# Performance work log

Measured on AMD Instinct MI355X. Metric: run time of the kernel, lower is better.

The kernel has to match this reference:

```python
import jax, jax.numpy as jnp
import numpy as np

NEG = -1e30  # log-space 'zero' (stand-in for log(0))


def setup_inputs() -> dict:
    key = jax.random.key(0)
    k1, k2 = jax.random.split(key)
    K, Tp1, Y = 4, 513, 256  # K feature fns, T+1 transition steps, Y labels
    f = jax.random.normal(k1, (K, Tp1, Y, Y), dtype=jnp.float32)
    w = jax.random.uniform(k2, (K,), dtype=jnp.float32)
    return {"f": f, "w": w}


def _crf_core(f, w):
    # logM[t] = sum_k w_k * f[k, t]  (log of the original M before exp)
    K, Tp1, Y, _ = f.shape
    T = Tp1 - 1
    logM = jnp.einsum('k,ktij->tij', w, f)  # [T+1, Y, Y]
    # Boundary masking (original zeros M[0,1:,:] and M[T,:,1:]):
    is0 = (jnp.arange(Y) == 0)
    logM = logM.at[0].set(jnp.where(is0[:, None], logM[0], NEG))
    logM = logM.at[T].set(jnp.where(is0[None, :], logM[T], NEG))

    # log-alpha forward scan (stable log-space form of alpha[i+1] = alpha[i] @ M[i])
    la0 = jnp.where(is0, 0.0, NEG)  # alpha[0] one-hot at label 0
    def fwd_step(la, lm):
        la_new = jax.nn.logsumexp(la[:, None] + lm, axis=0)
        return la_new, la_new
    _, las = jax.lax.scan(fwd_step, la0, logM)
    log_alpha = jnp.concatenate([la0[None], las], axis=0)  # [T+2, Y]

    # log-beta backward scan (beta[i] = M[i] @ beta[i+1])
    lbT = jnp.where(is0, 0.0, NEG)  # beta[T+1] one-hot at label 0
    def bwd_step(lb, lm):
        lb_new = jax.nn.logsumexp(lm + lb[None, :], axis=1)
        return lb_new, lb_new
    _, lbs = jax.lax.scan(bwd_step, lbT, logM, reverse=True)
    log_beta = jnp.concatenate([lbs, lbT[None]], axis=0)  # [T+2, Y]

    logZ = jax.nn.logsumexp(log_alpha[T + 1])
    # pairwise posterior p(y_{i}=y', y_{i+1}=y | x) = alpha_i * M_i * beta_{i+1} / Z
    p12 = jnp.exp(log_alpha[:-1][:, :, None] + logM + log_beta[1:][:, None, :] - logZ)
    return p12, logM


def _viterbi(logM):
    # delta[0] = logM[0, 0]; delta[i] = max_{y'} delta[i-1][y'] + logM[i][y', y]
    T = logM.shape[0] - 1
    def vit_step(d, lm):
        scores = d[:, None] + lm  # [Y, Y]
        return jnp.max(scores, axis=0), jnp.argmax(scores, axis=0)
    dT, idxs = jax.lax.scan(vit_step, logM[0, 0], logM[1:T])
    last = jnp.argmax(dT)
    def back_step(y, idx):
        yp = idx[y]
        return yp, yp
    _, prevs = jax.lax.scan(back_step, last, idxs, reverse=True)
    return jnp.concatenate([prevs, last[None]])  # [T]


def reference(f, w):
    p12, logM = _crf_core(f, w)
    path = _viterbi(logM)
    return p12, path
```

## Files before the change

kernel.cpp:

```cpp
#include <hip/hip_runtime.h>

#define NEGV (-1e30f)
#define NM   ((size_t)513*65536)
#define NF4  (NM/4)

typedef _Float16 h2 __attribute__((ext_vector_type(2)));

#if defined(__has_builtin)
#if __has_builtin(__builtin_amdgcn_fdot2)
#define HAS_FDOT2 1
#endif
#endif

__device__ __forceinline__ float dot2f(h2 a, h2 b, float c){
#ifdef HAS_FDOT2
  return __builtin_amdgcn_fdot2(a, b, c, false);
#else
  return c + (float)a.x*(float)b.x + (float)a.y*(float)b.y;
#endif
}

__device__ __forceinline__ h2 u2h2(unsigned u){ return __builtin_bit_cast(h2, u); }

struct WS {
  float *fA, *fB, *fD, *fLZ;
  _Float16 *hA, *hB;
  unsigned char* idx8;
  unsigned long long *flagF8, *flagB8;
  int *flagV, *ctr;
};
__device__ __forceinline__ WS get_ws(void* w){
  WS s;
  float* f = (float*)w;
  s.fA  = f;
  s.fB  = f + 131584;
  s.fD  = s.fB + 131584;
  s.fLZ = s.fD + 131072;
  s.hA  = (_Float16*)(s.fLZ + 64);
  s.hB  = s.hA + 131584;
  s.idx8 = (unsigned char*)(s.hB + 131584);
  s.flagF8 = (unsigned long long*)(s.idx8 + 131072);
  s.flagB8 = s.flagF8 + 576;
  s.flagV  = (int*)(s.flagB8 + 576);
  s.ctr    = s.flagV + 576;
  return s;
}

__device__ __forceinline__ float block_max256(float v, float* sred){
  #pragma unroll
  for (int m2=32;m2>0;m2>>=1) v = fmaxf(v, __shfl_xor(v, m2, 64));
  if ((threadIdx.x & 63)==0) sred[threadIdx.x>>6] = v;
  __syncthreads();
  return fmaxf(fmaxf(sred[0],sred[1]), fmaxf(sred[2],sred[3]));
}
__device__ __forceinline__ float block_sum256(float v, float* sred){
  #pragma unroll
  for (int m2=32;m2>0;m2>>=1) v += __shfl_xor(v, m2, 64);
  if ((threadIdx.x & 63)==0) sred[4+(threadIdx.x>>6)] = v;
  __syncthreads();
  return sred[4]+sred[5]+sred[6]+sred[7];
}

__global__ __launch_bounds__(1024) void k0_init(void* wsv){
  WS s = get_ws(wsv);
  const int tid = threadIdx.x;
  for (int i=tid;i<576;i+=1024){ s.flagF8[i]=0ull; s.flagB8[i]=0ull; s.flagV[i]=0; }
  if (tid < 64) s.ctr[tid] = 0;
  __syncthreads();
  if (tid < 256){
    s.fA[tid] = (tid==0)?0.0f:NEGV;
    s.hA[tid] = (tid==0)?(_Float16)1.0f:(_Float16)0.0f;
    s.fB[(size_t)513*256+tid] = (tid==0)?0.0f:NEGV;
    s.hB[(size_t)513*256+tid] = (tid==0)?(_Float16)1.0f:(_Float16)0.0f;
  }
  if (tid==0){ s.flagF8[0] = (1ull<<32); s.flagB8[513] = (1ull<<32); }
}

__global__ __launch_bounds__(1024) void k1_logM(const float* __restrict__ f,
                                                const float* __restrict__ w,
                                                float* __restrict__ lm, void* wsv){
  WS s = get_ws(wsv);
  const float w0=w[0], w1=w[1], w2=w[2], w3=w[3];
  const float4* f0=(const float4*)f;
  const float4* f1=f0+NF4; const float4* f2=f1+NF4; const float4* f3=f2+NF4;
  float4* o=(float4*)lm;
  for (size_t i=(size_t)blockIdx.x*1024+threadIdx.x; i<NF4; i+=(size_t)gridDim.x*1024){
    float4 a=f0[i], b=f1[i], c=f2[i], d=f3[i];
    float4 v;
    v.x = w0*a.x+w1*b.x+w2*c.x+w3*d.x;
    v.y = w0*a.y+w1*b.y+w2*c.y+w3*d.y;
    v.z = w0*a.z+w1*b.z+w2*c.z+w3*d.z;
    v.w = w0*a.w+w1*b.w+w2*c.w+w3*d.w;
    size_t e=i*4;
    int t=(int)(e>>16), r=(int)((e>>8)&255), cc=(int)(e&255);
    if (t==0 && r!=0){ v.x=NEGV; v.y=NEGV; v.z=NEGV; v.w=NEGV; }
    if (t==512){ if (cc!=0) v.x=NEGV; v.y=NEGV; v.z=NEGV; v.w=NEGV; }
    o[i]=v;
  }
  if (blockIdx.x==0 && threadIdx.x<256){
    int j=threadIdx.x;
    float sv = w0*f[j] + w1*f[NM+j] + w2*f[2*NM+j] + w3*f[3*NM+j];
    s.fD[j]=sv;
    if (j==0) s.flagV[0]=1;
  }
}

__global__ __launch_bounds__(256,1) void chains_k(const float* __restrict__ lm, void* wsv){
  WS s = get_ws(wsv);
  __shared__ int s_t;
  __shared__ float s_bcast;
  __shared__ float sred[8];
  __shared__ __align__(16) unsigned aL32[128];
  __shared__ __align__(16) float dL[256];
  __shared__ __align__(16) float ldsM[32768];
  const int tid = threadIdx.x;
  const int role = blockIdx.x % 3;
  if (tid==0) s_t = atomicAdd(&s.ctr[role], 1);
  __syncthreads();
  const int tk = s_t;

  if (role==0){
    if (tk >= 513) return;
    const float* M = lm + (size_t)tk*65536;
    h2 P[128];
    #pragma unroll
    for (int h=0;h<128;h++){
      float x0 = M[(size_t)(2*h  )*256 + tid];
      float x1 = M[(size_t)(2*h+1)*256 + tid];
      h2 v; v.x=(_Float16)fminf(__expf(x0),60000.0f);
            v.y=(_Float16)fminf(__expf(x1),60000.0f);
      P[h]=v;
    }
    asm volatile("s_waitcnt vmcnt(0)" ::: "memory");
    unsigned* hA32 = (unsigned*)s.hA;
    if (tid<128){
      unsigned long long v;
      while ((unsigned)((v=__hip_atomic_load(&s.flagF8[tk],__ATOMIC_RELAXED,__HIP_MEMORY_SCOPE_AGENT))>>32)==0u)
        __builtin_amdgcn_s_sleep(1);
      asm volatile("" ::: "memory");
      if (tid==0) s_bcast = __uint_as_float((unsigned)v);
      aL32[tid] = __hip_atomic_load(hA32 + (size_t)tk*128 + tid,
                                    __ATOMIC_RELAXED, __HIP_MEMORY_SCOPE_AGENT);
    }
    __syncthreads();
    const float ma = s_bcast;
    float ac0=0.0f, ac1=0.0f, ac2=0.0f, ac3=0.0f;
    const uint4* a4 = (const uint4*)aL32;
    #pragma unroll
    for (int q=0;q<32;q++){
      uint4 av = a4[q];
      ac0 = dot2f(P[4*q+0], u2h2(av.x), ac0);
      ac1 = dot2f(P[4*q+1], u2h2(av.y), ac1);
      ac2 = dot2f(P[4*q+2], u2h2(av.z), ac2);
      ac3 = dot2f(P[4*q+3], u2h2(av.w), ac3);
    }
    float alpha = ma + __logf((ac0+ac1)+(ac2+ac3));
    s.fA[(size_t)(tk+1)*256 + tid] = alpha;
    float m = block_max256(alpha, sred);
    float e = __expf(alpha - m);
    unsigned short hu = __builtin_bit_cast(unsigned short, (_Float16)e);
    unsigned po = (unsigned)__shfl_xor((int)hu, 1, 64);
    if ((tid&1)==0)
      __hip_atomic_store(hA32 + (size_t)(tk+1)*128 + (tid>>1),
                         (unsigned)hu | (po<<16),
                         __ATOMIC_RELAXED, __HIP_MEMORY_SCOPE_AGENT);
    if (tk==512){
      float sm = block_sum256(e, sred);
      if (tid==0) s.fLZ[0] = m + __logf(sm);
    }
    __syncthreads();
    if (tid==0)
      __hip_atomic_store(&s.flagF8[tk+1],
                         ((unsigned long long)1<<32) | (unsigned long long)__float_as_uint(m),
                         __ATOMIC_RELAXED, __HIP_MEMORY_SCOPE_AGENT);

  } else if (role==1){
    if (tk >= 513) return;
    const int tt = 512 - tk;
    const float* M = lm + (size_t)tt*65536;
    const float2* r2 = (const float2*)(M + (size_t)tid*256);
    h2 P[128];
    #pragma unroll
    for (int h=0;h<128;h++){
      float2 x = r2[h];
      h2 v; v.x=(_Float16)fminf(__expf(x.x),60000.0f);
            v.y=(_Float16)fminf(__expf(x.y),60000.0f);
      P[h]=v;
    }
    asm volatile("s_waitcnt vmcnt(0)" ::: "memory");
    unsigned* hB32 = (unsigned*)s.hB;
    if (tid<128){
      unsigned long long v;
      while ((unsigned)((v=__hip_atomic_load(&s.flagB8[tt+1],__ATOMIC_RELAXED,__HIP_MEMORY_SCOPE_AGENT))>>32)==0u)
        __builtin_amdgcn_s_sleep(1);
      asm volatile("" ::: "memory");
      if (tid==0) s_bcast = __uint_as_float((unsigned)v);
      aL32[tid] = __hip_atomic_load(hB32 + (size_t)(tt+1)*128 + tid,
                                    __ATOMIC_RELAXED, __HIP_MEMORY_SCOPE_AGENT);
    }
    __syncthreads();
    const float mb = s_bcast;
    float ac0=0.0f, ac1=0.0f, ac2=0.0f, ac3=0.0f;
    const uint4* a4 = (const uint4*)aL32;
    #pragma unroll
    for (int q=0;q<32;q++){
      uint4 av = a4[q];
      ac0 = dot2f(P[4*q+0], u2h2(av.x), ac0);
      ac1 = dot2f(P[4*q+1], u2h2(av.y), ac1);
      ac2 = dot2f(P[4*q+2], u2h2(av.z), ac2);
      ac3 = dot2f(P[4*q+3], u2h2(av.w), ac3);
    }
    float lbv = mb + __logf((ac0+ac1)+(ac2+ac3));
    s.fB[(size_t)tt*256 + tid] = lbv;
    float m = block_max256(lbv, sred);
    float e = __expf(lbv - m);
    unsigned short hu = __builtin_bit_cast(unsigned short, (_Float16)e);
    unsigned po = (unsigned)__shfl_xor((int)hu, 1, 64);
    if ((tid&1)==0)
      __hip_atomic_store(hB32 + (size_t)tt*128 + (tid>>1),
                         (unsigned)hu | (po<<16),
                         __ATOMIC_RELAXED, __HIP_MEMORY_SCOPE_AGENT);
    __syncthreads();
    if (tid==0)
      __hip_atomic_store(&s.flagB8[tt],
                         ((unsigned long long)1<<32) | (unsigned long long)__float_as_uint(m),
                         __ATOMIC_RELAXED, __HIP_MEMORY_SCOPE_AGENT);

  } else {
    if (tk >= 511) return;
    const float* M = lm + (size_t)(tk+1)*65536;
    float Pa[128];
    #pragma unroll
    for (int i=0;i<128;i++) Pa[i] = M[(size_t)i*256 + tid];
    {
      const float4* g4 = (const float4*)(M + 32768);
      float4* l4 = (float4*)ldsM;
      #pragma unroll
      for (int q=0;q<32;q++) l4[q*256 + tid] = g4[q*256 + tid];
    }
    asm volatile("s_waitcnt vmcnt(0)" ::: "memory");
    while (__hip_atomic_load(&s.flagV[tk],__ATOMIC_RELAXED,__HIP_MEMORY_SCOPE_AGENT)==0)
      __builtin_amdgcn_s_sleep(1);
    asm volatile("" ::: "memory");
    dL[tid] = __hip_atomic_load(s.fD + (size_t)tk*256 + tid,
                                __ATOMIC_RELAXED, __HIP_MEMORY_SCOPE_AGENT);
    __syncthreads();
    const float4* d4 = (const float4*)dL;
    float b0=-3.0e38f, b1=-3.0e38f, b2=-3.0e38f, b3=-3.0e38f;
    #pragma unroll
    for (int q=0;q<32;q++){
      float4 dv = d4[q];
      b0 = fmaxf(b0, dv.x + Pa[4*q+0]);
      b1 = fmaxf(b1, dv.y + Pa[4*q+1]);
      b2 = fmaxf(b2, dv.z + Pa[4*q+2]);
      b3 = fmaxf(b3, dv.w + Pa[4*q+3]);
    }
    #pragma unroll
    for (int q=0;q<32;q++){
      float4 dv = d4[32+q];
      b0 = fmaxf(b0, dv.x + ldsM[(4*q+0)*256 + tid]);
      b1 = fmaxf(b1, dv.y + ldsM[(4*q+1)*256 + tid]);
      b2 = fmaxf(b2, dv.z + ldsM[(4*q+2)*256 + tid]);
      b3 = fmaxf(b3, dv.w + ldsM[(4*q+3)*256 + tid]);
    }
    float best = fmaxf(fmaxf(b0,b1),fmaxf(b2,b3));
    __hip_atomic_store(s.fD + (size_t)(tk+1)*256 + tid, best,
                       __ATOMIC_RELAXED, __HIP_MEMORY_SCOPE_AGENT);
    __syncthreads();
    if (tid==0)
      __hip_atomic_store(&s.flagV[tk+1], 1, __ATOMIC_RELAXED, __HIP_MEMORY_SCOPE_AGENT);
    int bi = 0;
    #pragma unroll
    for (int r=127;r>=0;r--){ float v = dL[128+r] + ldsM[r*256 + tid]; bi = (v==best)? 128+r : bi; }
    #pragma unroll
    for (int i=127;i>=0;i--){ float v = dL[i] + Pa[i]; bi = (v==best)? i : bi; }
    s.idx8[(size_t)tk*256 + tid] = (unsigned char)bi;
  }
}

__global__ __launch_bounds__(1024) void k3_epilogue(float* __restrict__ pm, void* wsv,
                                                    float* __restrict__ pathOut){
  WS s = get_ws(wsv);
  __shared__ unsigned char sidx[65280];
  __shared__ int s_y;
  if (blockIdx.x == 0){
    const int tid = threadIdx.x;
    for (int i=tid;i<255*256;i+=1024) sidx[i] = s.idx8[(size_t)256*256 + i];
    __syncthreads();
    if (tid==0){
      const float* dT = s.fD + (size_t)511*256;
      float best = dT[0]; int last = 0;
      for (int j=1;j<256;j++){ float v=dT[j]; if (v>best){best=v;last=j;} }
      pathOut[511] = (float)last;
      int y = last;
      for (int rr=510;rr>=256;rr--){ y = sidx[(rr-256)*256 + y]; pathOut[rr]=(float)y; }
      s_y = y;
    }
    __syncthreads();
    for (int i=tid;i<255*256;i+=1024) sidx[i] = s.idx8[256 + i];
    __syncthreads();
    if (tid==0){
      int y = s_y;
      for (int rr=255;rr>=1;rr--){ y = sidx[(rr-1)*256 + y]; pathOut[rr]=(float)y; }
      y = s.idx8[y];
      pathOut[0] = (float)y;
    }
    return;
  }
  const float lz = s.fLZ[0];
  for (size_t i=(size_t)(blockIdx.x-1)*1024+threadIdx.x; i<NF4; i+=(size_t)(gridDim.x-1)*1024){
    size_t e = i*4;
    int t=(int)(e>>16), r=(int)((e>>8)&255), cc=(int)(e&255);
    float la = s.fA[(size_t)t*256 + r];
    float4 lb4 = *(const float4*)(s.fB + (size_t)(t+1)*256 + cc);
    float4 m4 = ((const float4*)pm)[i];
    float base = la - lz;
    float4 o;
    o.x = __expf(base + m4.x + lb4.x);
    o.y = __expf(base + m4.y + lb4.y);
    o.z = __expf(base + m4.z + lb4.z);
    o.w = __expf(base + m4.w + lb4.w);
    ((float4*)pm)[i] = o;
  }
}

extern "C" void kernel_launch(void* const* d_in, const int* in_sizes, int n_in,
                              void* d_out, int out_size, void* d_ws, size_t ws_size,
                              hipStream_t stream){
  const float* f = (const float*)d_in[0];
  const float* w = (const float*)d_in[1];
  float* out  = (float*)d_out;
  float* lm   = out;
  float* path = out + (out_size - 512);
  hipLaunchKernelGGL(k0_init,   dim3(1),    dim3(1024), 0, stream, d_ws);
  hipLaunchKernelGGL(k1_logM,   dim3(8208), dim3(1024), 0, stream, f, w, lm, d_ws);
  hipLaunchKernelGGL(chains_k,  dim3(1539), dim3(256),  0, stream, lm, d_ws);
  hipLaunchKernelGGL(k3_epilogue, dim3(8209), dim3(1024), 0, stream, lm, d_ws, path);
}
```

Measured before the change: 3.392 ms.

## Replace flag handshakes with sentinel-filled data polling in the sequential chains

Consumers of the forward, backward and Viterbi chains now spin directly on the payload words, which are pre-filled with an all-ones sentinel, instead of waiting on a separate ready flag and then loading the data. The producer's trailing block barrier before the flag store is removed, and the alpha and beta max flags are published right after the block max. Together these shorten the critical path of each serial step by removing one barrier and one flag round trip. The init kernel now runs on 128 blocks to fill the sentinel arrays, and correctness depends on no real payload ever matching the sentinel bit pattern.

New measurement: 3.105 ms. -8.5%, faster.

```diff
diff --git a/kernel.cpp b/kernel.cpp
--- a/kernel.cpp
+++ b/kernel.cpp
@@ -3,6 +3,7 @@
 #define NEGV (-1e30f)
 #define NM   ((size_t)513*65536)
 #define NF4  (NM/4)
+#define SENT 0xFFFFFFFFu
 
 typedef _Float16 h2 __attribute__((ext_vector_type(2)));
 
@@ -63,17 +64,26 @@
 
 __global__ __launch_bounds__(1024) void k0_init(void* wsv){
   WS s = get_ws(wsv);
-  const int tid = threadIdx.x;
-  for (int i=tid;i<576;i+=1024){ s.flagF8[i]=0ull; s.flagB8[i]=0ull; s.flagV[i]=0; }
-  if (tid < 64) s.ctr[tid] = 0;
-  __syncthreads();
-  if (tid < 256){
-    s.fA[tid] = (tid==0)?0.0f:NEGV;
-    s.hA[tid] = (tid==0)?(_Float16)1.0f:(_Float16)0.0f;
-    s.fB[(size_t)513*256+tid] = (tid==0)?0.0f:NEGV;
-    s.hB[(size_t)513*256+tid] = (tid==0)?(_Float16)1.0f:(_Float16)0.0f;
-  }
-  if (tid==0){ s.flagF8[0] = (1ull<<32); s.flagB8[513] = (1ull<<32); }
+  unsigned* hA32 = (unsigned*)s.hA;
+  unsigned* hB32 = (unsigned*)s.hB;
+  unsigned* fD32 = (unsigned*)s.fD;
+  const size_t g = (size_t)blockIdx.x*1024 + threadIdx.x;
+  const size_t stride = (size_t)gridDim.x*1024;
+  for (size_t i=g; i<65664;  i+=stride) hA32[128+i] = SENT;
+  for (size_t i=g; i<65664;  i+=stride) hB32[i]     = SENT;
+  for (size_t i=g; i<130816; i+=stride) fD32[256+i] = SENT;
+  if (blockIdx.x==0){
+    const int tid = threadIdx.x;
+    for (int i=tid;i<576;i+=1024){ s.flagF8[i]=0ull; s.flagB8[i]=0ull; }
+    if (tid < 64) s.ctr[tid] = 0;
+    if (tid < 256){
+      s.fA[tid] = (tid==0)?0.0f:NEGV;
+      s.hA[tid] = (tid==0)?(_Float16)1.0f:(_Float16)0.0f;
+      s.fB[(size_t)513*256+tid] = (tid==0)?0.0f:NEGV;
+      s.hB[(size_t)513*256+tid] = (tid==0)?(_Float16)1.0f:(_Float16)0.0f;
+    }
+    if (tid==0){ s.flagF8[0] = (1ull<<32); s.flagB8[513] = (1ull<<32); }
+  }
 }
 
 __global__ __launch_bounds__(1024) void k1_logM(const float* __restrict__ f,
@@ -101,7 +111,6 @@
     int j=threadIdx.x;
     float sv = w0*f[j] + w1*f[NM+j] + w2*f[2*NM+j] + w3*f[3*NM+j];
     s.fD[j]=sv;
-    if (j==0) s.flagV[0]=1;
   }
 }
 
@@ -134,13 +143,20 @@
     asm volatile("s_waitcnt vmcnt(0)" ::: "memory");
     unsigned* hA32 = (unsigned*)s.hA;
     if (tid<128){
-      unsigned long long v;
-      while ((unsigned)((v=__hip_atomic_load(&s.flagF8[tk],__ATOMIC_RELAXED,__HIP_MEMORY_SCOPE_AGENT))>>32)==0u)
-        __builtin_amdgcn_s_sleep(1);
-      asm volatile("" ::: "memory");
-      if (tid==0) s_bcast = __uint_as_float((unsigned)v);
-      aL32[tid] = __hip_atomic_load(hA32 + (size_t)tk*128 + tid,
-                                    __ATOMIC_RELAXED, __HIP_MEMORY_SCOPE_AGENT);
+      const unsigned* mp = hA32 + (size_t)tk*128 + tid;
+      unsigned mv = __hip_atomic_load(mp,__ATOMIC_RELAXED,__HIP_MEMORY_SCOPE_AGENT);
+      while (mv==SENT){
+        __builtin_amdgcn_s_sleep(1);
+        mv = __hip_atomic_load(mp,__ATOMIC_RELAXED,__HIP_MEMORY_SCOPE_AGENT);
+      }
+      aL32[tid] = mv;
+    } else if (tid==128){
+      unsigned long long v = __hip_atomic_load(&s.flagF8[tk],__ATOMIC_RELAXED,__HIP_MEMORY_SCOPE_AGENT);
+      while ((unsigned)(v>>32)==0u){
+        __builtin_amdgcn_s_sleep(1);
+        v = __hip_atomic_load(&s.flagF8[tk],__ATOMIC_RELAXED,__HIP_MEMORY_SCOPE_AGENT);
+      }
+      s_bcast = __uint_as_float((unsigned)v);
     }
     __syncthreads();
     const float ma = s_bcast;
@@ -157,6 +173,10 @@
     float alpha = ma + __logf((ac0+ac1)+(ac2+ac3));
     s.fA[(size_t)(tk+1)*256 + tid] = alpha;
     float m = block_max256(alpha, sred);
+    if (tid==0)
+      __hip_atomic_store(&s.flagF8[tk+1],
+                         ((unsigned long long)1<<32) | (unsigned long long)__float_as_uint(m),
+                         __ATOMIC_RELAXED, __HIP_MEMORY_SCOPE_AGENT);
     float e = __expf(alpha - m);
     unsigned short hu = __builtin_bit_cast(unsigned short, (_Float16)e);
     unsigned po = (unsigned)__shfl_xor((int)hu, 1, 64);
@@ -168,11 +188,6 @@
       float sm = block_sum256(e, sred);
       if (tid==0) s.fLZ[0] = m + __logf(sm);
     }
-    __syncthreads();
-    if (tid==0)
-      __hip_atomic_store(&s.flagF8[tk+1],
-                         ((unsigned long long)1<<32) | (unsigned long long)__float_as_uint(m),
-                         __ATOMIC_RELAXED, __HIP_MEMORY_SCOPE_AGENT);
 
   } else if (role==1){
     if (tk >= 513) return;
@@ -190,13 +205,20 @@
     asm volatile("s_waitcnt vmcnt(0)" ::: "memory");
     unsigned* hB32 = (unsigned*)s.hB;
     if (tid<128){
-      unsigned long long v;
-      while ((unsigned)((v=__hip_atomic_load(&s.flagB8[tt+1],__ATOMIC_RELAXED,__HIP_MEMORY_SCOPE_AGENT))>>32)==0u)
-        __builtin_amdgcn_s_sleep(1);
-      asm volatile("" ::: "memory");
-      if (tid==0) s_bcast = __uint_as_float((unsigned)v);
-      aL32[tid] = __hip_atomic_load(hB32 + (size_t)(tt+1)*128 + tid,
-                                    __ATOMIC_RELAXED, __HIP_MEMORY_SCOPE_AGENT);
+      const unsigned* mp = hB32 + (size_t)(tt+1)*128 + tid;
+      unsigned mv = __hip_atomic_load(mp,__ATOMIC_RELAXED,__HIP_MEMORY_SCOPE_AGENT);
+      while (mv==SENT){
+        __builtin_amdgcn_s_sleep(1);
+        mv = __hip_atomic_load(mp,__ATOMIC_RELAXED,__HIP_MEMORY_SCOPE_AGENT);
+      }
+      aL32[tid] = mv;
+    } else if (tid==128){
+      unsigned long long v = __hip_atomic_load(&s.flagB8[tt+1],__ATOMIC_RELAXED,__HIP_MEMORY_SCOPE_AGENT);
+      while ((unsigned)(v>>32)==0u){
+        __builtin_amdgcn_s_sleep(1);
+        v = __hip_atomic_load(&s.flagB8[tt+1],__ATOMIC_RELAXED,__HIP_MEMORY_SCOPE_AGENT);
+      }
+      s_bcast = __uint_as_float((unsigned)v);
     }
     __syncthreads();
     const float mb = s_bcast;
@@ -213,6 +235,10 @@
     float lbv = mb + __logf((ac0+ac1)+(ac2+ac3));
     s.fB[(size_t)tt*256 + tid] = lbv;
     float m = block_max256(lbv, sred);
+    if (tid==0)
+      __hip_atomic_store(&s.flagB8[tt],
+                         ((unsigned long long)1<<32) | (unsigned long long)__float_as_uint(m),
+                         __ATOMIC_RELAXED, __HIP_MEMORY_SCOPE_AGENT);
     float e = __expf(lbv - m);
     unsigned short hu = __builtin_bit_cast(unsigned short, (_Float16)e);
     unsigned po = (unsigned)__shfl_xor((int)hu, 1, 64);
@@ -220,11 +246,6 @@
       __hip_atomic_store(hB32 + (size_t)tt*128 + (tid>>1),
                          (unsigned)hu | (po<<16),
                          __ATOMIC_RELAXED, __HIP_MEMORY_SCOPE_AGENT);
-    __syncthreads();
-    if (tid==0)
-      __hip_atomic_store(&s.flagB8[tt],
-                         ((unsigned long long)1<<32) | (unsigned long long)__float_as_uint(m),
-                         __ATOMIC_RELAXED, __HIP_MEMORY_SCOPE_AGENT);
 
   } else {
     if (tk >= 511) return;
@@ -239,11 +260,15 @@
       for (int q=0;q<32;q++) l4[q*256 + tid] = g4[q*256 + tid];
     }
     asm volatile("s_waitcnt vmcnt(0)" ::: "memory");
-    while (__hip_atomic_load(&s.flagV[tk],__ATOMIC_RELAXED,__HIP_MEMORY_SCOPE_AGENT)==0)
-      __builtin_amdgcn_s_sleep(1);
-    asm volatile("" ::: "memory");
-    dL[tid] = __hip_atomic_load(s.fD + (size_t)tk*256 + tid,
-                                __ATOMIC_RELAXED, __HIP_MEMORY_SCOPE_AGENT);
+    {
+      const unsigned* dp = (const unsigned*)s.fD + (size_t)tk*256 + tid;
+      unsigned dv = __hip_atomic_load(dp,__ATOMIC_RELAXED,__HIP_MEMORY_SCOPE_AGENT);
+      while (dv==SENT){
+        __builtin_amdgcn_s_sleep(1);
+        dv = __hip_atomic_load(dp,__ATOMIC_RELAXED,__HIP_MEMORY_SCOPE_AGENT);
+      }
+      dL[tid] = __uint_as_float(dv);
+    }
     __syncthreads();
     const float4* d4 = (const float4*)dL;
     float b0=-3.0e38f, b1=-3.0e38f, b2=-3.0e38f, b3=-3.0e38f;
@@ -264,11 +289,9 @@
       b3 = fmaxf(b3, dv.w + ldsM[(4*q+3)*256 + tid]);
     }
     float best = fmaxf(fmaxf(b0,b1),fmaxf(b2,b3));
-    __hip_atomic_store(s.fD + (size_t)(tk+1)*256 + tid, best,
+    __hip_atomic_store((unsigned*)s.fD + (size_t)(tk+1)*256 + tid,
+                       __float_as_uint(best),
                        __ATOMIC_RELAXED, __HIP_MEMORY_SCOPE_AGENT);
-    __syncthreads();
-    if (tid==0)
-      __hip_atomic_store(&s.flagV[tk+1], 1, __ATOMIC_RELAXED, __HIP_MEMORY_SCOPE_AGENT);
     int bi = 0;
     #pragma unroll
     for (int r=127;r>=0;r--){ float v = dL[128+r] + ldsM[r*256 + tid]; bi = (v==best)? 128+r : bi; }
@@ -332,7 +355,7 @@
   float* out  = (float*)d_out;
   float* lm   = out;
   float* path = out + (out_size - 512);
-  hipLaunchKernelGGL(k0_init,   dim3(1),    dim3(1024), 0, stream, d_ws);
+  hipLaunchKernelGGL(k0_init,   dim3(128),  dim3(1024), 0, stream, d_ws);
   hipLaunchKernelGGL(k1_logM,   dim3(8208), dim3(1024), 0, stream, f, w, lm, d_ws);
   hipLaunchKernelGGL(chains_k,  dim3(1539), dim3(256),  0, stream, lm, d_ws);
   hipLaunchKernelGGL(k3_epilogue, dim3(8209), dim3(1024), 0, stream, lm, d_ws, path);
```
